# Kernel tuning notes

Measured on AMD Instinct MI355X. Metric: run time of the kernel, lower is better.

Reference implementation:

```python
import jax, jax.numpy as jnp
import numpy as np

B_SZ = 512; S = 3; F = 5; C = 62; E = 5
D_MODEL = C * E * F          # 1550
N_LAYERS = 2
D_STATE = 16
EXPAND = 2
D_CONV = 4
ED = EXPAND * D_MODEL        # 3100
DT_RANK = (D_MODEL + 15) // 16  # 97
VOCAB = 128
EPS = 1e-5


def setup_inputs() -> dict:
    key = jax.random.key(0)
    ks = jax.random.split(key, 10)
    def g(i, shape, scale=0.02):
        return jax.random.normal(ks[i], shape, dtype=jnp.float32) * scale
    A_log = jnp.tile(jnp.log(jnp.arange(1, D_STATE + 1, dtype=jnp.float32))[None, None, :],
                     (N_LAYERS, ED, 1))
    return {
        "x": jax.random.normal(ks[0], (B_SZ, S, F, C, E), dtype=jnp.float32),
        "in_proj_w": g(1, (N_LAYERS, 2 * ED, D_MODEL)),
        "conv_w": g(2, (N_LAYERS, ED, 1, D_CONV), 0.1),
        "conv_b": jnp.zeros((N_LAYERS, ED), jnp.float32),
        "x_proj_w": g(3, (N_LAYERS, DT_RANK + 2 * D_STATE, ED)),
        "dt_proj_w": g(4, (N_LAYERS, ED, DT_RANK), 0.1),
        "dt_proj_b": jnp.full((N_LAYERS, ED), -4.6, jnp.float32),  # softplus ~ 0.01
        "A_log": A_log,
        "D_param": jnp.ones((N_LAYERS, ED), jnp.float32),
        "out_proj_w": g(5, (N_LAYERS, D_MODEL, ED)),
        "norm_w": jnp.ones((N_LAYERS, D_MODEL), jnp.float32),
        "normf_w": jnp.ones((D_MODEL,), jnp.float32),
        "lm_head_w": g(6, (VOCAB, D_MODEL)),
        "bn_w": jnp.ones((F,), jnp.float32),
        "bn_b": jnp.zeros((F,), jnp.float32),
        "emb_w": g(7, (256, VOCAB)),
        "emb_b": jnp.zeros((256,), jnp.float32),
    }


def _rmsnorm(x, w):
    return x * jax.lax.rsqrt(jnp.mean(x * x, axis=-1, keepdims=True) + EPS) * w


def _silu(x):
    return x * jax.nn.sigmoid(x)


def _causal_conv(xt, w, b):
    # xt: (B, ED, L); w: (ED, 1, K) depthwise causal conv (pad K-1 left)
    y = jax.lax.conv_general_dilated(xt, w, (1,), [(D_CONV - 1, 0)],
                                     feature_group_count=ED)
    return y + b[None, :, None]


def _ssm_scan(deltaA, deltaBx, Cm):
    # deltaA, deltaBx: (B, L, ED, N); Cm: (B, L, N)
    def step(h, inp):
        dA, dBx, c = inp
        h = dA * h + dBx                      # (B, ED, N)
        y = jnp.einsum('ben,bn->be', h, c)    # (B, ED)
        return h, y
    h0 = jnp.zeros((deltaA.shape[0], ED, D_STATE), deltaA.dtype)
    xs = (deltaA.transpose(1, 0, 2, 3), deltaBx.transpose(1, 0, 2, 3), Cm.transpose(1, 0, 2))
    _, ys = jax.lax.scan(step, h0, xs)
    return ys.transpose(1, 0, 2)              # (B, L, ED)


def _mixer(h, in_w, cw, cb, xp_w, dt_w, dt_b, A_log, Dp, out_w):
    # h: (B, L, D_MODEL)
    xz = jnp.einsum('bld,ed->ble', h, in_w)   # (B, L, 2*ED)
    x_in, z = jnp.split(xz, 2, axis=-1)
    xc = _silu(_causal_conv(x_in.transpose(0, 2, 1), cw, cb).transpose(0, 2, 1))  # (B,L,ED)
    dbc = jnp.einsum('ble,re->blr', xc, xp_w)  # (B, L, DT_RANK + 2N)
    dt = dbc[..., :DT_RANK]
    Bm = dbc[..., DT_RANK:DT_RANK + D_STATE]
    Cm = dbc[..., DT_RANK + D_STATE:]
    delta = jax.nn.softplus(jnp.einsum('blr,er->ble', dt, dt_w) + dt_b)  # (B,L,ED)
    A = -jnp.exp(A_log)                       # (ED, N)
    deltaA = jnp.exp(delta[..., None] * A)                       # (B,L,ED,N)
    deltaBx = delta[..., None] * Bm[:, :, None, :] * xc[..., None]
    y = _ssm_scan(deltaA, deltaBx, Cm) + Dp * xc
    return jnp.einsum('ble,de->bld', y * _silu(z), out_w)


def reference(x, in_proj_w, conv_w, conv_b, x_proj_w, dt_proj_w, dt_proj_b,
              A_log, D_param, out_proj_w, norm_w, normf_w, lm_head_w,
              bn_w, bn_b, emb_w, emb_b):
    b, s, f, c, e = x.shape
    fx = x.transpose(0, 1, 3, 2, 4).reshape(b, s, c * f * e)  # (B, S, D_MODEL)
    h = fx
    for l in range(N_LAYERS):
        h = h + _mixer(_rmsnorm(h, norm_w[l]), in_proj_w[l], conv_w[l], conv_b[l],
                       x_proj_w[l], dt_proj_w[l], dt_proj_b[l], A_log[l],
                       D_param[l], out_proj_w[l])
    h = _rmsnorm(h, normf_w)
    logits = jnp.einsum('bsd,vd->bsv', h, lm_head_w)          # (B, S, 128)
    m = jnp.broadcast_to(logits[:, None], (b, f, s, VOCAB))    # repeat over f
    # BatchNorm2d(feature_dim) in training mode: stats over (B, S, VOCAB) per channel f
    mean = jnp.mean(m, axis=(0, 2, 3), keepdims=True)
    var = jnp.var(m, axis=(0, 2, 3), keepdims=True)
    mn = (m - mean) * jax.lax.rsqrt(var + EPS)
    mn = mn * bn_w[None, :, None, None] + bn_b[None, :, None, None]
    return jnp.einsum('bfsv,ov->bfso', mn, emb_w) + emb_b      # (B, F, S, 256)
```

## Files before the change

### kernel.cpp

```cpp
#include <hip/hip_runtime.h>
#include <hip/hip_bf16.h>
#include <math.h>

#define B_SZ 512
#define SEQ 3
#define D_MODEL 1550
#define ED 3100
#define NSTATE 16
#define DTR 97
#define DBC_R 129
#define VOCAB 128
#define NBS (B_SZ*SEQ)
#define EPSV 1e-5f

#define KD 1600
#define KE 3136
#define NIP 6272
#define NXP 256
#define NOP 1664
#define NDT 3200
#define KDT 128
#define DBC_LD 256

#define QIP 2508800
#define QXP 200704
#define QDT 102400
#define QOP 1304576
#define AEL 49600
#define QLM 51200
#define TEL 32768
#define PREP_N1 4166080
#define PREP_N0 4250306

static inline int cdiv_h(int a, int b){ return (a + b - 1) / b; }

__device__ __forceinline__ float silu_f(float x){ return x / (1.0f + expf(-x)); }

using bf16x8 = __attribute__((ext_vector_type(8))) short;
using f32x4  = __attribute__((ext_vector_type(4))) float;

__device__ __forceinline__ void gload16(const void* g, void* l){
  __builtin_amdgcn_global_load_lds(
      (const __attribute__((address_space(1))) unsigned int*)g,
      (__attribute__((address_space(3))) unsigned int*)l,
      16, 0, 0);
}

__device__ __forceinline__ unsigned short bfbits(float v){
  __hip_bfloat16 b = __float2bfloat16(v);
  return *(unsigned short*)&b;
}

__global__ void k_permute(const float* __restrict__ x, float* __restrict__ h){
  int idx = blockIdx.x * 256 + threadIdx.x;
  if (idx >= NBS * D_MODEL) return;
  int d = idx % D_MODEL;
  int row = idx / D_MODEL;
  int e = d % 5;
  int f = (d / 5) % 5;
  int c = d / 25;
  h[idx] = x[(((size_t)row * 5 + f) * 62 + c) * 5 + e];
}

__device__ __forceinline__ void cast4(const float* __restrict__ src,
                                      __hip_bfloat16* __restrict__ dst,
                                      int q, int N, int K, int Kp){
  int i4 = q * 4;
  int row = i4 / Kp;
  int col = i4 % Kp;
  const float* srow = src + (size_t)row * K;
  ushort4 o;
  o.x = bfbits((row < N && col + 0 < K) ? srow[col + 0] : 0.f);
  o.y = bfbits((row < N && col + 1 < K) ? srow[col + 1] : 0.f);
  o.z = bfbits((row < N && col + 2 < K) ? srow[col + 2] : 0.f);
  o.w = bfbits((row < N && col + 3 < K) ? srow[col + 3] : 0.f);
  *(ushort4*)(dst + i4) = o;
}

__global__ __launch_bounds__(256)
void k_prep(const float* __restrict__ ipw, const float* __restrict__ xpw,
            const float* __restrict__ dtw, const float* __restrict__ opw,
            const float* __restrict__ alog,
            const float* __restrict__ lmw, const float* __restrict__ embw,
            __hip_bfloat16* __restrict__ ipb, __hip_bfloat16* __restrict__ xpb,
            __hip_bfloat16* __restrict__ dtwb, __hip_bfloat16* __restrict__ opb,
            float* __restrict__ A_t,
            __hip_bfloat16* __restrict__ lmb,
            float* __restrict__ emb_t, float* __restrict__ sumw,
            float* __restrict__ stats, int l0){
  int idx = blockIdx.x * 256 + threadIdx.x;
  if (idx < QIP){ cast4(ipw, ipb, idx, 2 * ED, D_MODEL, KD); return; } idx -= QIP;
  if (idx < QXP){ cast4(xpw, xpb, idx, DBC_R, ED, KE); return; } idx -= QXP;
  if (idx < QDT){ cast4(dtw, dtwb, idx, ED, DTR, KDT); return; } idx -= QDT;
  if (idx < QOP){ cast4(opw, opb, idx, D_MODEL, ED, KE); return; } idx -= QOP;
  if (idx < AEL){
    int n = idx / ED, ch = idx % ED;
    A_t[idx] = -expf(alog[(size_t)ch * NSTATE + n]);
    return;
  } idx -= AEL;
  if (!l0) return;
  if (idx < QLM){ cast4(lmw, lmb, idx, VOCAB, D_MODEL, KD); return; } idx -= QLM;
  if (idx < TEL){
    int v = idx >> 8, o = idx & 255;
    emb_t[idx] = embw[(size_t)o * VOCAB + v];
    return;
  } idx -= TEL;
  if (idx < 256){
    const float* r = embw + (size_t)idx * VOCAB;
    float s = 0.f;
    for (int v = 0; v < VOCAB; v++) s += r[v];
    sumw[idx] = s;
    return;
  } idx -= 256;
  if (idx < 2) stats[idx] = 0.f;
}

__global__ void k_rmsnorm_bf16(const float* __restrict__ in, const float* __restrict__ w,
                               __hip_bfloat16* __restrict__ out, int D, int Kp){
  int row = blockIdx.x;
  const float* xr = in + (size_t)row * D;
  float ss = 0.f;
  for (int i = threadIdx.x; i < D; i += blockDim.x){ float v = xr[i]; ss = fmaf(v, v, ss); }
  __shared__ float red[4];
  __shared__ float sscale;
  int lane = threadIdx.x & 63, wv = threadIdx.x >> 6;
  #pragma unroll
  for (int o = 32; o > 0; o >>= 1) ss += __shfl_down(ss, o, 64);
  if (lane == 0) red[wv] = ss;
  __syncthreads();
  if (threadIdx.x == 0){
    float t = red[0] + red[1] + red[2] + red[3];
    sscale = 1.0f / sqrtf(t / (float)D + EPSV);
  }
  __syncthreads();
  float sc = sscale;
  __hip_bfloat16* orow = out + (size_t)row * Kp;
  for (int i = threadIdx.x; i < Kp; i += blockDim.x){
    float v = (i < D) ? xr[i] * sc * w[i] : 0.f;
    orow[i] = __float2bfloat16(v);
  }
}

template<int SPLITS, bool OUT_BF16, bool PARTIAL>
__global__ __launch_bounds__(256)
void k_gemm2(const __hip_bfloat16* __restrict__ A, const __hip_bfloat16* __restrict__ B,
             void* Cv, int Kp, int Nld, int Nreal){
  __shared__ short Al[2][4096];
  __shared__ short Bl[2][4096];
  const int gx = gridDim.x, gy = gridDim.y;
  const int nwg = gx * gy;
  const int wg = blockIdx.y * gx + blockIdx.x;
  const int q = nwg >> 3, r = nwg & 7;
  const int xcd = wg & 7, off = wg >> 3;
  const int nid = (xcd < r ? xcd * (q + 1) : r * (q + 1) + (xcd - r) * q) + off;
  const int bm = (nid % gy) * 128;
  const int bn = (nid / gy) * 128;

  const int t = threadIdx.x;
  const int tt8 = t * 8;

  int kb = 0, ke = Kp;
  if (SPLITS > 1){
    int Kc = ((Kp / SPLITS + 31) / 32) * 32;
    kb = blockIdx.z * Kc;
    ke = min(kb + Kc, Kp);
    if (kb >= ke) return;
  }
  const int nt = (ke - kb) / 32;

  const int cg = ((t & 3) ^ ((t >> 2) & 3)) * 8;
  const short* Ab = (const short*)A;
  const short* Bb = (const short*)B;
  const short* ga0 = Ab + (size_t)(bm + (t >> 2)) * Kp + cg;
  const short* ga1 = Ab + (size_t)(bm + 64 + (t >> 2)) * Kp + cg;
  const short* gb0 = Bb + (size_t)(bn + (t >> 2)) * Kp + cg;
  const short* gb1 = Bb + (size_t)(bn + 64 + (t >> 2)) * Kp + cg;

  const int l = t & 63;
  const int wid = t >> 6;
  const int wr = wid >> 1, wc = wid & 1;
  const int fr = l & 15;
  const int cc = ((l >> 4) ^ (l & 3)) * 8;

  f32x4 acc[4][4] = {};

#define STAGE(buf, kof) do{ \
    gload16(ga0 + (kof), &Al[buf][tt8]); \
    gload16(ga1 + (kof), &Al[buf][2048 + tt8]); \
    gload16(gb0 + (kof), &Bl[buf][tt8]); \
    gload16(gb1 + (kof), &Bl[buf][2048 + tt8]); }while(0)

  STAGE(0, kb);
  __syncthreads();
  int cur = 0;
  for (int it = 0; it < nt; ++it){
    if (it + 1 < nt) STAGE(cur ^ 1, kb + (it + 1) * 32);
    bf16x8 af[4], bfr[4];
    #pragma unroll
    for (int m = 0; m < 4; m++)
      af[m] = *(const bf16x8*)&Al[cur][(wr * 64 + m * 16 + fr) * 32 + cc];
    #pragma unroll
    for (int n = 0; n < 4; n++)
      bfr[n] = *(const bf16x8*)&Bl[cur][(wc * 64 + n * 16 + fr) * 32 + cc];
    #pragma unroll
    for (int m = 0; m < 4; m++)
      #pragma unroll
      for (int n = 0; n < 4; n++)
        acc[m][n] = __builtin_amdgcn_mfma_f32_16x16x32_bf16(af[m], bfr[n], acc[m][n], 0, 0, 0);
    if (it + 1 < nt){ __syncthreads(); cur ^= 1; }
  }
#undef STAGE

  float* Cf = (float*)Cv;
  __hip_bfloat16* Cb = (__hip_bfloat16*)Cv;
  if (PARTIAL){
    const size_t pstride = (size_t)gy * 128 * Nld;
    if (OUT_BF16) Cb += (size_t)blockIdx.z * pstride;
    else          Cf += (size_t)blockIdx.z * pstride;
  }
  const int r0 = (l >> 4) * 4;
  #pragma unroll
  for (int m = 0; m < 4; m++){
    #pragma unroll
    for (int n = 0; n < 4; n++){
      int col = bn + wc * 64 + n * 16 + fr;
      if (col < Nreal){
        size_t base = (size_t)(bm + wr * 64 + m * 16 + r0) * Nld + col;
        #pragma unroll
        for (int j = 0; j < 4; j++){
          float v = acc[m][n][j];
          size_t o = base + (size_t)j * Nld;
          if (OUT_BF16) Cb[o] = __float2bfloat16(v);
          else          Cf[o] = v;
        }
      }
    }
  }
}

__global__ void k_conv_silu(const __hip_bfloat16* __restrict__ xz, const float* __restrict__ cw,
                            const float* __restrict__ cb, __hip_bfloat16* __restrict__ xc_b){
  int idx = blockIdx.x * 256 + threadIdx.x;
  if (idx >= B_SZ * KE) return;
  int ch = idx % KE;
  int b  = idx / KE;
  size_t ob = (size_t)b * SEQ * KE + ch;
  if (ch >= ED){
    __hip_bfloat16 z = __float2bfloat16(0.f);
    xc_b[ob] = z; xc_b[ob + KE] = z; xc_b[ob + 2 * KE] = z;
    return;
  }
  const __hip_bfloat16* base = xz + (size_t)b * SEQ * NIP + ch;
  float x0 = __bfloat162float(base[0]);
  float x1 = __bfloat162float(base[NIP]);
  float x2 = __bfloat162float(base[2 * NIP]);
  const float* w = cw + (size_t)ch * 4;
  float w1 = w[1], w2 = w[2], w3 = w[3];
  float bb = cb[ch];
  float s0 = silu_f(fmaf(w3, x0, bb));
  float s1 = silu_f(fmaf(w2, x0, fmaf(w3, x1, bb)));
  float s2 = silu_f(fmaf(w1, x0, fmaf(w2, x1, fmaf(w3, x2, bb))));
  xc_b[ob]          = __float2bfloat16(s0);
  xc_b[ob + KE]     = __float2bfloat16(s1);
  xc_b[ob + 2 * KE] = __float2bfloat16(s2);
}

__global__ __launch_bounds__(256)
void k_xred(const float* __restrict__ part, float* __restrict__ dbc,
            __hip_bfloat16* __restrict__ dbc_b){
  int idx = blockIdx.x * 256 + threadIdx.x;
  if (idx >= NBS * DBC_LD) return;
  float s = 0.f;
  #pragma unroll
  for (int p = 0; p < 8; p++) s += part[(size_t)p * NBS * DBC_LD + idx];
  dbc[idx] = s;
  int c = idx & 255, row = idx >> 8;
  if (c < KDT) dbc_b[(size_t)row * KDT + c] = __float2bfloat16(c < DTR ? s : 0.f);
}

__global__ __launch_bounds__(256)
void k_ored(const __hip_bfloat16* __restrict__ part, float* __restrict__ h){
  int idx = blockIdx.x * 256 + threadIdx.x;
  if (idx >= NBS * D_MODEL) return;
  float s = h[idx];
  #pragma unroll
  for (int p = 0; p < 4; p++)
    s += __bfloat162float(part[(size_t)p * NBS * D_MODEL + idx]);
  h[idx] = s;
}

__global__ __launch_bounds__(256)
void k_scan2(const __hip_bfloat16* __restrict__ delta_b, const float* __restrict__ dbc,
             const float* __restrict__ dtb, const float* __restrict__ A_t,
             const float* __restrict__ Dp, const __hip_bfloat16* __restrict__ xz,
             __hip_bfloat16* __restrict__ xc_b){
  __shared__ float sB[SEQ][NSTATE], sC[SEQ][NSTATE];
  int b = blockIdx.y;
  if (threadIdx.x < SEQ * 2 * NSTATE){
    int t = threadIdx.x / (2 * NSTATE), r = threadIdx.x % (2 * NSTATE);
    float v = dbc[(size_t)(b * SEQ + t) * DBC_LD + DTR + r];
    if (r < NSTATE) sB[t][r] = v; else sC[t][r - NSTATE] = v;
  }
  __syncthreads();
  int ch = blockIdx.x * 256 + threadIdx.x;
  if (ch >= ED) return;

  float bias = dtb[ch];
  float dlt[SEQ];
  #pragma unroll
  for (int t = 0; t < SEQ; t++){
    float acc = __bfloat162float(delta_b[(size_t)(b * SEQ + t) * NDT + ch]) + bias;
    dlt[t] = (acc > 20.f) ? acc : log1pf(expf(acc));
  }

  size_t ob = (size_t)b * SEQ * KE + ch;
  float xcv[SEQ] = { __bfloat162float(xc_b[ob]),
                     __bfloat162float(xc_b[ob + KE]),
                     __bfloat162float(xc_b[ob + 2 * KE]) };
  float y[SEQ] = {0.f, 0.f, 0.f};
  #pragma unroll
  for (int n = 0; n < NSTATE; n++){
    float Av = A_t[(size_t)n * ED + ch];
    float hs = 0.f;
    #pragma unroll
    for (int t = 0; t < SEQ; t++){
      float dA = expf(dlt[t] * Av);
      hs = fmaf(dA, hs, dlt[t] * sB[t][n] * xcv[t]);
      y[t] = fmaf(hs, sC[t][n], y[t]);
    }
  }
  float dp = Dp[ch];
  const __hip_bfloat16* zbase = xz + (size_t)b * SEQ * NIP + ED + ch;
  #pragma unroll
  for (int t = 0; t < SEQ; t++){
    float z = __bfloat162float(zbase[(size_t)t * NIP]);
    float yy = fmaf(dp, xcv[t], y[t]);
    xc_b[ob + (size_t)t * KE] = __float2bfloat16(yy * silu_f(z));
  }
}

__global__ __launch_bounds__(256)
void k_statsred(const float* __restrict__ part, float* __restrict__ logits,
                float* __restrict__ stats){
  float s = 0.f, ss = 0.f;
  for (int i = blockIdx.x * 256 + threadIdx.x; i < NBS * VOCAB; i += gridDim.x * 256){
    float v = 0.f;
    #pragma unroll
    for (int p = 0; p < 4; p++) v += part[(size_t)p * NBS * VOCAB + i];
    logits[i] = v;
    s += v; ss = fmaf(v, v, ss);
  }
  #pragma unroll
  for (int o = 32; o > 0; o >>= 1){ s += __shfl_down(s, o, 64); ss += __shfl_down(ss, o, 64); }
  __shared__ float rs[4], rss[4];
  int lane = threadIdx.x & 63, wv = threadIdx.x >> 6;
  if (lane == 0){ rs[wv] = s; rss[wv] = ss; }
  __syncthreads();
  if (threadIdx.x == 0){
    atomicAdd(&stats[0], rs[0] + rs[1] + rs[2] + rs[3]);
    atomicAdd(&stats[1], rss[0] + rss[1] + rss[2] + rss[3]);
  }
}

__global__ __launch_bounds__(256)
void k_projfinal(const float* __restrict__ logits, const float* __restrict__ emb_t,
                 const float* __restrict__ sumw, const float* __restrict__ stats,
                 const float* __restrict__ bnw, const float* __restrict__ bnb,
                 const float* __restrict__ embb, float* __restrict__ out){
  __shared__ float row[VOCAB];
  int r = blockIdx.x;
  int o = threadIdx.x;
  if (o < VOCAB) row[o] = logits[(size_t)r * VOCAB + o];
  __syncthreads();
  float p = 0.f;
  #pragma unroll 8
  for (int v = 0; v < VOCAB; v++) p = fmaf(row[v], emb_t[v * 256 + o], p);
  const float invN = 1.0f / (float)(NBS * VOCAB);
  float mean = stats[0] * invN;
  float var  = stats[1] * invN - mean * mean;
  float rstd = rsqrtf(var + EPSV);
  int b = r / SEQ, s = r % SEQ;
  float sw = sumw[o];
  float base = rstd * (p - mean * sw);
  float eb = embb[o];
  #pragma unroll
  for (int f = 0; f < 5; f++){
    out[(((size_t)(b * 5 + f)) * SEQ + s) * 256 + o] = bnw[f] * base + bnb[f] * sw + eb;
  }
}

extern "C" void kernel_launch(void* const* d_in, const int* in_sizes, int n_in,
                              void* d_out, int out_size, void* d_ws, size_t ws_size,
                              hipStream_t stream) {
  const float* x          = (const float*)d_in[0];
  const float* in_proj_w  = (const float*)d_in[1];
  const float* conv_w     = (const float*)d_in[2];
  const float* conv_b     = (const float*)d_in[3];
  const float* x_proj_w   = (const float*)d_in[4];
  const float* dt_proj_w  = (const float*)d_in[5];
  const float* dt_proj_b  = (const float*)d_in[6];
  const float* A_log      = (const float*)d_in[7];
  const float* D_param    = (const float*)d_in[8];
  const float* out_proj_w = (const float*)d_in[9];
  const float* norm_w     = (const float*)d_in[10];
  const float* normf_w    = (const float*)d_in[11];
  const float* lm_head_w  = (const float*)d_in[12];
  const float* bn_w       = (const float*)d_in[13];
  const float* bn_b       = (const float*)d_in[14];
  const float* emb_w      = (const float*)d_in[15];
  const float* emb_b      = (const float*)d_in[16];

  float* ws = (float*)d_ws;
  float* h      = ws;
  float* dbc    = h      + (size_t)NBS * D_MODEL;
  float* logits = dbc    + (size_t)NBS * DBC_LD;
  float* sumw   = logits + (size_t)NBS * VOCAB;
  float* stats  = sumw   + 256;
  float* A_t    = stats  + 2;
  float* emb_t  = A_t    + (size_t)NSTATE * ED;
  float* spart  = emb_t  + (size_t)VOCAB * 256;
  size_t spart_f = ((size_t)4 * NBS * D_MODEL * 2 + 3) / 4;
  float* xpart  = spart;
  float* lmpart = spart;
  __hip_bfloat16* opart = (__hip_bfloat16*)spart;
  __hip_bfloat16* xz_b   = (__hip_bfloat16*)(spart + spart_f);
  __hip_bfloat16* hn_b   = xz_b   + (size_t)NBS * NIP;
  __hip_bfloat16* xc_b   = hn_b   + (size_t)NBS * KD;
  __hip_bfloat16* dbc_b  = xc_b   + (size_t)NBS * KE;
  __hip_bfloat16* dlt_b  = dbc_b  + (size_t)NBS * KDT;
  __hip_bfloat16* ipb    = dlt_b  + (size_t)NBS * NDT;
  __hip_bfloat16* xpb    = ipb    + (size_t)NIP * KD;
  __hip_bfloat16* dtwb   = xpb    + (size_t)NXP * KE;
  __hip_bfloat16* opb    = dtwb   + (size_t)NDT * KDT;
  __hip_bfloat16* lmb    = opb    + (size_t)NOP * KE;
  size_t need = (size_t)((char*)(lmb + (size_t)VOCAB * KD) - (char*)ws);
  if (ws_size < need) return;

  k_permute<<<cdiv_h(NBS * D_MODEL, 256), 256, 0, stream>>>(x, h);

  for (int l = 0; l < 2; l++){
    const float* ipw = in_proj_w  + (size_t)l * 2 * ED * D_MODEL;
    const float* cw  = conv_w     + (size_t)l * ED * 4;
    const float* cb  = conv_b     + (size_t)l * ED;
    const float* xpw = x_proj_w   + (size_t)l * DBC_R * ED;
    const float* dtw = dt_proj_w  + (size_t)l * ED * DTR;
    const float* dtb = dt_proj_b  + (size_t)l * ED;
    const float* al  = A_log      + (size_t)l * ED * NSTATE;
    const float* dp  = D_param    + (size_t)l * ED;
    const float* opw = out_proj_w + (size_t)l * D_MODEL * ED;
    const float* nw  = norm_w     + (size_t)l * D_MODEL;

    k_prep<<<cdiv_h(l == 0 ? PREP_N0 : PREP_N1, 256), 256, 0, stream>>>(
        ipw, xpw, dtw, opw, al, lm_head_w, emb_w,
        ipb, xpb, dtwb, opb, A_t, lmb, emb_t, sumw, stats, l == 0 ? 1 : 0);

    k_rmsnorm_bf16<<<NBS, 256, 0, stream>>>(h, nw, hn_b, D_MODEL, KD);

    k_gemm2<1, true, false><<<dim3(NIP / 128, NBS / 128, 1), 256, 0, stream>>>(
        hn_b, ipb, xz_b, KD, NIP, NIP);

    k_conv_silu<<<cdiv_h(B_SZ * KE, 256), 256, 0, stream>>>(xz_b, cw, cb, xc_b);

    k_gemm2<8, false, true><<<dim3(NXP / 128, NBS / 128, 8), 256, 0, stream>>>(
        xc_b, xpb, xpart, KE, DBC_LD, DBC_LD);
    k_xred<<<cdiv_h(NBS * DBC_LD, 256), 256, 0, stream>>>(xpart, dbc, dbc_b);

    k_gemm2<1, true, false><<<dim3(NDT / 128, NBS / 128, 1), 256, 0, stream>>>(
        dbc_b, dtwb, dlt_b, KDT, NDT, NDT);

    k_scan2<<<dim3(cdiv_h(ED, 256), B_SZ), 256, 0, stream>>>(
        dlt_b, dbc, dtb, A_t, dp, xz_b, xc_b);

    k_gemm2<4, true, true><<<dim3(NOP / 128, NBS / 128, 4), 256, 0, stream>>>(
        xc_b, opb, opart, KE, D_MODEL, D_MODEL);
    k_ored<<<cdiv_h(NBS * D_MODEL, 256), 256, 0, stream>>>(opart, h);
  }

  k_rmsnorm_bf16<<<NBS, 256, 0, stream>>>(h, normf_w, hn_b, D_MODEL, KD);
  k_gemm2<4, false, true><<<dim3(1, NBS / 128, 4), 256, 0, stream>>>(
      hn_b, lmb, lmpart, KD, VOCAB, VOCAB);
  k_statsred<<<192, 256, 0, stream>>>(lmpart, logits, stats);

  k_projfinal<<<NBS, 256, 0, stream>>>(logits, emb_t, sumw, stats,
                                       bn_w, bn_b, emb_b, (float*)d_out);
}
```

Measured before the change: 497.8 us.

## Fuse permute/residual-reduce into RMSNorm and split-K the in_proj GEMM

The input permute is merged with the first RMSNorm, and the out_proj partial-sum reduction plus residual add is merged with the following RMSNorm. This removes separate elementwise passes over the hidden state and several kernel launches. The in_proj GEMM now runs split-K=2, with the second half written to a separate bf16 buffer. The conv/silu kernel sums the two halves, and also writes the summed z half back in place. That doubles the in_proj workgroup count for better occupancy, at the cost of extra bf16 traffic and an extra bf16 rounding of the partial sums.

Measured after the change: 492.1 us. Within noise of the previous version (-1.1%).

```diff
diff --git a/kernel.cpp b/kernel.cpp
--- a/kernel.cpp
+++ b/kernel.cpp
@@ -51,15 +51,79 @@
   return *(unsigned short*)&b;
 }
 
-__global__ void k_permute(const float* __restrict__ x, float* __restrict__ h){
-  int idx = blockIdx.x * 256 + threadIdx.x;
-  if (idx >= NBS * D_MODEL) return;
-  int d = idx % D_MODEL;
-  int row = idx / D_MODEL;
-  int e = d % 5;
-  int f = (d / 5) % 5;
-  int c = d / 25;
-  h[idx] = x[(((size_t)row * 5 + f) * 62 + c) * 5 + e];
+__global__ __launch_bounds__(256)
+void k_perm_rms(const float* __restrict__ x, const float* __restrict__ w,
+                float* __restrict__ h, __hip_bfloat16* __restrict__ hn){
+  int row = blockIdx.x;
+  const float* xr = x + (size_t)row * D_MODEL;
+  float vreg[7]; int dreg[7];
+  int cnt = 0;
+  float ss = 0.f;
+  for (int i = threadIdx.x; i < D_MODEL; i += 256){
+    float v = xr[i];
+    int e = i % 5, c = (i / 5) % 62, f = i / 310;
+    int d = (c * 5 + f) * 5 + e;
+    vreg[cnt] = v; dreg[cnt] = d; cnt++;
+    ss = fmaf(v, v, ss);
+    h[(size_t)row * D_MODEL + d] = v;
+  }
+  __shared__ float red[4];
+  __shared__ float sscale;
+  int lane = threadIdx.x & 63, wv = threadIdx.x >> 6;
+  #pragma unroll
+  for (int o = 32; o > 0; o >>= 1) ss += __shfl_down(ss, o, 64);
+  if (lane == 0) red[wv] = ss;
+  __syncthreads();
+  if (threadIdx.x == 0){
+    float t = red[0] + red[1] + red[2] + red[3];
+    sscale = 1.0f / sqrtf(t / (float)D_MODEL + EPSV);
+  }
+  __syncthreads();
+  float sc = sscale;
+  __hip_bfloat16* orow = hn + (size_t)row * KD;
+  for (int k = 0; k < cnt; k++)
+    orow[dreg[k]] = __float2bfloat16(vreg[k] * sc * w[dreg[k]]);
+  for (int i = D_MODEL + threadIdx.x; i < KD; i += 256)
+    orow[i] = __float2bfloat16(0.f);
+}
+
+__global__ __launch_bounds__(256)
+void k_rms_res(float* __restrict__ h, const __hip_bfloat16* __restrict__ part,
+               const float* __restrict__ w, __hip_bfloat16* __restrict__ hn){
+  int row = blockIdx.x;
+  size_t hb = (size_t)row * D_MODEL;
+  float vreg[7];
+  int cnt = 0;
+  float ss = 0.f;
+  for (int i = threadIdx.x; i < D_MODEL; i += 256){
+    float v = h[hb + i];
+    #pragma unroll
+    for (int p = 0; p < 4; p++)
+      v += __bfloat162float(part[(size_t)p * NBS * D_MODEL + hb + i]);
+    h[hb + i] = v;
+    vreg[cnt++] = v;
+    ss = fmaf(v, v, ss);
+  }
+  __shared__ float red[4];
+  __shared__ float sscale;
+  int lane = threadIdx.x & 63, wv = threadIdx.x >> 6;
+  #pragma unroll
+  for (int o = 32; o > 0; o >>= 1) ss += __shfl_down(ss, o, 64);
+  if (lane == 0) red[wv] = ss;
+  __syncthreads();
+  if (threadIdx.x == 0){
+    float t = red[0] + red[1] + red[2] + red[3];
+    sscale = 1.0f / sqrtf(t / (float)D_MODEL + EPSV);
+  }
+  __syncthreads();
+  float sc = sscale;
+  __hip_bfloat16* orow = hn + (size_t)row * KD;
+  for (int k = 0; k < cnt; k++){
+    int i = threadIdx.x + k * 256;
+    orow[i] = __float2bfloat16(vreg[k] * sc * w[i]);
+  }
+  for (int i = D_MODEL + threadIdx.x; i < KD; i += 256)
+    orow[i] = __float2bfloat16(0.f);
 }
 
 __device__ __forceinline__ void cast4(const float* __restrict__ src,
@@ -115,36 +179,10 @@
   if (idx < 2) stats[idx] = 0.f;
 }
 
-__global__ void k_rmsnorm_bf16(const float* __restrict__ in, const float* __restrict__ w,
-                               __hip_bfloat16* __restrict__ out, int D, int Kp){
-  int row = blockIdx.x;
-  const float* xr = in + (size_t)row * D;
-  float ss = 0.f;
-  for (int i = threadIdx.x; i < D; i += blockDim.x){ float v = xr[i]; ss = fmaf(v, v, ss); }
-  __shared__ float red[4];
-  __shared__ float sscale;
-  int lane = threadIdx.x & 63, wv = threadIdx.x >> 6;
-  #pragma unroll
-  for (int o = 32; o > 0; o >>= 1) ss += __shfl_down(ss, o, 64);
-  if (lane == 0) red[wv] = ss;
-  __syncthreads();
-  if (threadIdx.x == 0){
-    float t = red[0] + red[1] + red[2] + red[3];
-    sscale = 1.0f / sqrtf(t / (float)D + EPSV);
-  }
-  __syncthreads();
-  float sc = sscale;
-  __hip_bfloat16* orow = out + (size_t)row * Kp;
-  for (int i = threadIdx.x; i < Kp; i += blockDim.x){
-    float v = (i < D) ? xr[i] * sc * w[i] : 0.f;
-    orow[i] = __float2bfloat16(v);
-  }
-}
-
-template<int SPLITS, bool OUT_BF16, bool PARTIAL>
+template<int SPLITS, bool OUT_BF16, bool PARTIAL, bool DUAL>
 __global__ __launch_bounds__(256)
 void k_gemm2(const __hip_bfloat16* __restrict__ A, const __hip_bfloat16* __restrict__ B,
-             void* Cv, int Kp, int Nld, int Nreal){
+             void* Cv, void* Cv1, int Kp, int Nld, int Nreal){
   __shared__ short Al[2][4096];
   __shared__ short Bl[2][4096];
   const int gx = gridDim.x, gy = gridDim.y;
@@ -213,6 +251,7 @@
 
   float* Cf = (float*)Cv;
   __hip_bfloat16* Cb = (__hip_bfloat16*)Cv;
+  if (DUAL && blockIdx.z == 1) Cb = (__hip_bfloat16*)Cv1;
   if (PARTIAL){
     const size_t pstride = (size_t)gy * 128 * Nld;
     if (OUT_BF16) Cb += (size_t)blockIdx.z * pstride;
@@ -238,8 +277,10 @@
   }
 }
 
-__global__ void k_conv_silu(const __hip_bfloat16* __restrict__ xz, const float* __restrict__ cw,
-                            const float* __restrict__ cb, __hip_bfloat16* __restrict__ xc_b){
+__global__ void k_conv_silu2(__hip_bfloat16* __restrict__ xz0,
+                             const __hip_bfloat16* __restrict__ xz1,
+                             const float* __restrict__ cw, const float* __restrict__ cb,
+                             __hip_bfloat16* __restrict__ xc_b){
   int idx = blockIdx.x * 256 + threadIdx.x;
   if (idx >= B_SZ * KE) return;
   int ch = idx % KE;
@@ -250,10 +291,19 @@
     xc_b[ob] = z; xc_b[ob + KE] = z; xc_b[ob + 2 * KE] = z;
     return;
   }
-  const __hip_bfloat16* base = xz + (size_t)b * SEQ * NIP + ch;
-  float x0 = __bfloat162float(base[0]);
-  float x1 = __bfloat162float(base[NIP]);
-  float x2 = __bfloat162float(base[2 * NIP]);
+  size_t rb = (size_t)b * SEQ * NIP;
+  const __hip_bfloat16* p0 = xz0 + rb + ch;
+  const __hip_bfloat16* p1 = xz1 + rb + ch;
+  float x0 = __bfloat162float(p0[0])       + __bfloat162float(p1[0]);
+  float x1 = __bfloat162float(p0[NIP])     + __bfloat162float(p1[NIP]);
+  float x2 = __bfloat162float(p0[2 * NIP]) + __bfloat162float(p1[2 * NIP]);
+  __hip_bfloat16* q0 = xz0 + rb + ED + ch;
+  const __hip_bfloat16* q1 = xz1 + rb + ED + ch;
+  #pragma unroll
+  for (int t = 0; t < SEQ; t++){
+    float zv = __bfloat162float(q0[(size_t)t * NIP]) + __bfloat162float(q1[(size_t)t * NIP]);
+    q0[(size_t)t * NIP] = __float2bfloat16(zv);
+  }
   const float* w = cw + (size_t)ch * 4;
   float w1 = w[1], w2 = w[2], w3 = w[3];
   float bb = cb[ch];
@@ -276,17 +326,6 @@
   dbc[idx] = s;
   int c = idx & 255, row = idx >> 8;
   if (c < KDT) dbc_b[(size_t)row * KDT + c] = __float2bfloat16(c < DTR ? s : 0.f);
-}
-
-__global__ __launch_bounds__(256)
-void k_ored(const __hip_bfloat16* __restrict__ part, float* __restrict__ h){
-  int idx = blockIdx.x * 256 + threadIdx.x;
-  if (idx >= NBS * D_MODEL) return;
-  float s = h[idx];
-  #pragma unroll
-  for (int p = 0; p < 4; p++)
-    s += __bfloat162float(part[(size_t)p * NBS * D_MODEL + idx]);
-  h[idx] = s;
 }
 
 __global__ __launch_bounds__(256)
@@ -419,10 +458,11 @@
   float* A_t    = stats  + 2;
   float* emb_t  = A_t    + (size_t)NSTATE * ED;
   float* spart  = emb_t  + (size_t)VOCAB * 256;
-  size_t spart_f = ((size_t)4 * NBS * D_MODEL * 2 + 3) / 4;
+  size_t spart_f = (size_t)NBS * NIP / 2;
   float* xpart  = spart;
   float* lmpart = spart;
   __hip_bfloat16* opart = (__hip_bfloat16*)spart;
+  __hip_bfloat16* ipz1  = (__hip_bfloat16*)spart;
   __hip_bfloat16* xz_b   = (__hip_bfloat16*)(spart + spart_f);
   __hip_bfloat16* hn_b   = xz_b   + (size_t)NBS * NIP;
   __hip_bfloat16* xc_b   = hn_b   + (size_t)NBS * KD;
@@ -436,8 +476,6 @@
   size_t need = (size_t)((char*)(lmb + (size_t)VOCAB * KD) - (char*)ws);
   if (ws_size < need) return;
 
-  k_permute<<<cdiv_h(NBS * D_MODEL, 256), 256, 0, stream>>>(x, h);
-
   for (int l = 0; l < 2; l++){
     const float* ipw = in_proj_w  + (size_t)l * 2 * ED * D_MODEL;
     const float* cw  = conv_w     + (size_t)l * ED * 4;
@@ -454,31 +492,34 @@
         ipw, xpw, dtw, opw, al, lm_head_w, emb_w,
         ipb, xpb, dtwb, opb, A_t, lmb, emb_t, sumw, stats, l == 0 ? 1 : 0);
 
-    k_rmsnorm_bf16<<<NBS, 256, 0, stream>>>(h, nw, hn_b, D_MODEL, KD);
-
-    k_gemm2<1, true, false><<<dim3(NIP / 128, NBS / 128, 1), 256, 0, stream>>>(
-        hn_b, ipb, xz_b, KD, NIP, NIP);
-
-    k_conv_silu<<<cdiv_h(B_SZ * KE, 256), 256, 0, stream>>>(xz_b, cw, cb, xc_b);
-
-    k_gemm2<8, false, true><<<dim3(NXP / 128, NBS / 128, 8), 256, 0, stream>>>(
-        xc_b, xpb, xpart, KE, DBC_LD, DBC_LD);
+    if (l == 0){
+      k_perm_rms<<<NBS, 256, 0, stream>>>(x, nw, h, hn_b);
+    } else {
+      k_rms_res<<<NBS, 256, 0, stream>>>(h, opart, nw, hn_b);
+    }
+
+    k_gemm2<2, true, false, true><<<dim3(NIP / 128, NBS / 128, 2), 256, 0, stream>>>(
+        hn_b, ipb, xz_b, ipz1, KD, NIP, NIP);
+
+    k_conv_silu2<<<cdiv_h(B_SZ * KE, 256), 256, 0, stream>>>(xz_b, ipz1, cw, cb, xc_b);
+
+    k_gemm2<8, false, true, false><<<dim3(NXP / 128, NBS / 128, 8), 256, 0, stream>>>(
+        xc_b, xpb, xpart, nullptr, KE, DBC_LD, DBC_LD);
     k_xred<<<cdiv_h(NBS * DBC_LD, 256), 256, 0, stream>>>(xpart, dbc, dbc_b);
 
-    k_gemm2<1, true, false><<<dim3(NDT / 128, NBS / 128, 1), 256, 0, stream>>>(
-        dbc_b, dtwb, dlt_b, KDT, NDT, NDT);
+    k_gemm2<1, true, false, false><<<dim3(NDT / 128, NBS / 128, 1), 256, 0, stream>>>(
+        dbc_b, dtwb, dlt_b, nullptr, KDT, NDT, NDT);
 
     k_scan2<<<dim3(cdiv_h(ED, 256), B_SZ), 256, 0, stream>>>(
         dlt_b, dbc, dtb, A_t, dp, xz_b, xc_b);
 
-    k_gemm2<4, true, true><<<dim3(NOP / 128, NBS / 128, 4), 256, 0, stream>>>(
-        xc_b, opb, opart, KE, D_MODEL, D_MODEL);
-    k_ored<<<cdiv_h(NBS * D_MODEL, 256), 256, 0, stream>>>(opart, h);
-  }
-
-  k_rmsnorm_bf16<<<NBS, 256, 0, stream>>>(h, normf_w, hn_b, D_MODEL, KD);
-  k_gemm2<4, false, true><<<dim3(1, NBS / 128, 4), 256, 0, stream>>>(
-      hn_b, lmb, lmpart, KD, VOCAB, VOCAB);
+    k_gemm2<4, true, true, false><<<dim3(NOP / 128, NBS / 128, 4), 256, 0, stream>>>(
+        xc_b, opb, opart, nullptr, KE, D_MODEL, D_MODEL);
+  }
+
+  k_rms_res<<<NBS, 256, 0, stream>>>(h, opart, normf_w, hn_b);
+  k_gemm2<4, false, true, false><<<dim3(1, NBS / 128, 4), 256, 0, stream>>>(
+      hn_b, lmb, lmpart, nullptr, KD, VOCAB, VOCAB);
   k_statsred<<<192, 256, 0, stream>>>(lmpart, logits, stats);
 
   k_projfinal<<<NBS, 256, 0, stream>>>(logits, emb_t, sumw, stats,
```
